# Performance work log

Measured on AMD Instinct MI355X. Metric: run time of the kernel, lower is better.

The kernel has to match this reference:

```python
import jax, jax.numpy as jnp
import numpy as np

B, S, D, H = 8, 1024, 256, 8


def setup_inputs() -> dict:
    key = jax.random.key(0)
    ks = jax.random.split(key, 8)
    scale = 0.02
    return {
        "x": jax.random.normal(ks[0], (B, S, D), dtype=jnp.float32),
        "Wq": jax.random.normal(ks[1], (H, D, D), dtype=jnp.float32) * scale,
        "Wk": jax.random.normal(ks[2], (H, D, D), dtype=jnp.float32) * scale,
        "Wv": jax.random.normal(ks[3], (H, D, D), dtype=jnp.float32) * scale,
        "bq": jax.random.normal(ks[4], (H, D), dtype=jnp.float32) * scale,
        "bk": jax.random.normal(ks[5], (H, D), dtype=jnp.float32) * scale,
        "bv": jax.random.normal(ks[6], (H, D), dtype=jnp.float32) * scale,
        "Wp": jax.random.normal(ks[7], (D, H * D), dtype=jnp.float32) * scale,
    }


def reference(x, Wq, Wk, Wv, bq, bk, bv, Wp):
    # Per-head Linear layers, vectorized over the head axis.
    # torch Linear: y = x @ W.T + b, W shape [out, in] -> einsum 'bsd,hed->bhse'
    q = jnp.einsum('bsd,hed->bhse', x, Wq) + bq[:, None, :]   # [B,H,S,D]
    k = jnp.einsum('bsd,hed->bhse', x, Wk) + bk[:, None, :]
    v = jnp.einsum('bsd,hed->bhse', x, Wv) + bv[:, None, :]
    d = x.shape[-1]
    scores = jnp.einsum('bhse,bhte->bhst', q, k) / jnp.sqrt(jnp.float32(d))
    attn = jax.nn.softmax(scores, axis=-1)                    # softmax over keys (dim=2 per head)
    o = jnp.einsum('bhst,bhte->bhse', attn, v)                # [B,H,S,D]
    # concat heads along feature dim (head order preserved)
    o = o.transpose(0, 2, 1, 3).reshape(x.shape[0], x.shape[1], -1)  # [B,S,H*D]
    return o @ Wp.T                                           # bias-free projection [B,S,D]
```

## Files before the change

kernel.cpp:

```cpp
#include <hip/hip_runtime.h>

typedef unsigned short u16;
typedef __attribute__((ext_vector_type(4)))  float f32x4;
typedef __attribute__((ext_vector_type(16))) float f32x16;
typedef __attribute__((ext_vector_type(8)))  short s16x8;
typedef __attribute__((ext_vector_type(4)))  unsigned short u16x4;

typedef const __attribute__((address_space(1))) void* gp1;
typedef __attribute__((address_space(3))) void* lp3;
#define GLOAD16(g, l) __builtin_amdgcn_global_load_lds((gp1)(g), (lp3)(l), 16, 0, 0)

__device__ __forceinline__ u16 f2bf(float f) {
    union { float f; unsigned u; } c; c.f = f;
    unsigned r = c.u + 0x7fffu + ((c.u >> 16) & 1u);
    return (u16)(r >> 16);
}

__global__ void castall(const float* __restrict__ x,  const float* __restrict__ wq,
                        const float* __restrict__ wk, const float* __restrict__ wv,
                        const float* __restrict__ wp,
                        u16* __restrict__ xb,  u16* __restrict__ wqb, u16* __restrict__ wkb,
                        u16* __restrict__ wvb, u16* __restrict__ wpb) {
    int blk = blockIdx.x;
    const float* src; u16* dst; long off;
    if (blk < 2048) { src = x; dst = xb; off = (long)blk * 1024; }
    else {
        int w = (blk - 2048) >> 9, bb = (blk - 2048) & 511;
        src = (w == 0 ? wq : w == 1 ? wk : w == 2 ? wv : wp);
        dst = (w == 0 ? wqb : w == 1 ? wkb : w == 2 ? wvb : wpb);
        off = (long)bb * 1024;
    }
    long i = off + threadIdx.x * 4;
    f32x4 v = *(const f32x4*)(src + i);
    u16x4 o;
    o[0] = f2bf(v[0]); o[1] = f2bf(v[1]); o[2] = f2bf(v[2]); o[3] = f2bf(v[3]);
    *(u16x4*)(dst + i) = o;
}

__global__ __launch_bounds__(256) void qkv_gemm(
    const u16* __restrict__ xb,
    const u16* __restrict__ Wqb, const u16* __restrict__ Wkb, const u16* __restrict__ Wvb,
    const float* __restrict__ bq, const float* __restrict__ bk, const float* __restrict__ bv,
    u16* __restrict__ Qb, u16* __restrict__ Kimg, u16* __restrict__ Vimg)
{
    __shared__ u16 As[128 * 32];
    __shared__ u16 Bs[128 * 32];
    const int tid  = threadIdx.x;
    const int lane = tid & 63;
    const int li   = lane & 15, lg = lane >> 4;
    const int wave = tid >> 6;
    const int wr   = wave >> 1, wc = wave & 1;
    const int m0   = blockIdx.x * 128;
    const int n0g  = blockIdx.y * 128;
    const int w    = n0g >> 11;
    const int h    = (n0g >> 8) & 7;
    const int e0   = n0g & 255;
    const u16* Wsel = (w == 0 ? Wqb : (w == 1 ? Wkb : Wvb)) + h * 65536;

    const int srow = tid >> 2;
    const int scol = (tid & 3) * 8;

    f32x4 acc[4][4] = {};

    for (int k0 = 0; k0 < 256; k0 += 32) {
        __syncthreads();
        #pragma unroll
        for (int i = 0; i < 2; ++i) {
            int row = i * 64 + srow;
            GLOAD16(&xb[(m0 + row) * 256 + k0 + scol],   &As[i * 2048 + tid * 8]);
            GLOAD16(&Wsel[(e0 + row) * 256 + k0 + scol], &Bs[i * 2048 + tid * 8]);
        }
        __syncthreads();
        s16x8 af[4], bf[4];
        #pragma unroll
        for (int mi = 0; mi < 4; ++mi)
            af[mi] = *(const s16x8*)&As[(wr * 64 + mi * 16 + li) * 32 + lg * 8];
        #pragma unroll
        for (int ni = 0; ni < 4; ++ni)
            bf[ni] = *(const s16x8*)&Bs[(wc * 64 + ni * 16 + li) * 32 + lg * 8];
        #pragma unroll
        for (int mi = 0; mi < 4; ++mi)
            #pragma unroll
            for (int ni = 0; ni < 4; ++ni)
                acc[mi][ni] = __builtin_amdgcn_mfma_f32_16x16x32_bf16(af[mi], bf[ni], acc[mi][ni], 0, 0, 0);
    }

    const int b  = m0 >> 10;
    const int s0 = m0 & 1023;
    if (w == 0) {
        const float* bp = bq + 256 * h;
        #pragma unroll
        for (int ni = 0; ni < 4; ++ni) {
            const int e = e0 + wc * 64 + ni * 16 + li;
            const float bias = bp[e];
            u16* obase = Qb + ((size_t)(b * 8 + h)) * 1024 * 256 + e;
            #pragma unroll
            for (int mi = 0; mi < 4; ++mi)
                #pragma unroll
                for (int r = 0; r < 4; ++r) {
                    int s = s0 + wr * 64 + mi * 16 + lg * 4 + r;
                    obase[(size_t)s * 256] = f2bf(acc[mi][ni][r] + bias);
                }
        }
    } else if (w == 1) {
        const float* bp = bk + 256 * h;
        u16* kb = Kimg + ((size_t)(b * 8 + h)) * 262144;
        #pragma unroll
        for (int ni = 0; ni < 4; ++ni) {
            const int e = e0 + wc * 64 + ni * 16 + li;
            const float bias = bp[e];
            #pragma unroll
            for (int mi = 0; mi < 4; ++mi)
                #pragma unroll
                for (int r = 0; r < 4; ++r) {
                    int s = s0 + wr * 64 + mi * 16 + lg * 4 + r;
                    int t = s >> 5, rr = s & 31;
                    size_t idx = (size_t)t * 8192 + rr * 256
                               + (((e & ~7) ^ ((rr & 7) << 3)) | (e & 7));
                    kb[idx] = f2bf(acc[mi][ni][r] + bias);
                }
        }
    } else {
        const float* bp = bv + 256 * h;
        u16* vb = Vimg + ((size_t)(b * 8 + h)) * 327680;
        #pragma unroll
        for (int ni = 0; ni < 4; ++ni) {
            const int e = e0 + wc * 64 + ni * 16 + li;
            const float bias = bp[e];
            #pragma unroll
            for (int mi = 0; mi < 4; ++mi) {
                int s = s0 + wr * 64 + mi * 16 + lg * 4;
                int t = s >> 5, cj = s & 31;
                size_t idx = (size_t)t * 10240 + e * 40 + cj;
                u16x4 pk;
                #pragma unroll
                for (int r = 0; r < 4; ++r) pk[r] = f2bf(acc[mi][ni][r] + bias);
                *(u16x4*)&vb[idx] = pk;
            }
        }
    }
}

__device__ __forceinline__ void softmax_pack(
    f32x16& sacc, float& m_run, float& l_run, f32x16* oacc,
    int hi, s16x8& paA, s16x8& paB)
{
    const float C = 0.09016844f;
    const float THR = 16.0f;
    float pm = -1e30f;
    #pragma unroll
    for (int r = 0; r < 16; ++r) pm = fmaxf(pm, sacc[r]);
    pm = fmaxf(pm, __shfl_xor(pm, 32));
    if (!__all(pm - m_run <= THR)) {
        const float mnew = fmaxf(m_run, pm);
        const float corr = __builtin_amdgcn_exp2f((m_run - mnew) * C);
        l_run *= corr;
        #pragma unroll
        for (int r = 0; r < 16; ++r) {
            float rc = __shfl(corr, (r & 3) + 8 * (r >> 2) + 4 * hi);
            #pragma unroll
            for (int et = 0; et < 8; ++et) oacc[et][r] *= rc;
        }
        m_run = mnew;
    }
    float psum = 0.f;
    #pragma unroll
    for (int r = 0; r < 16; ++r) {
        float p = __builtin_amdgcn_exp2f((sacc[r] - m_run) * C);
        psum += p;
        sacc[r] = p;
    }
    psum += __shfl_xor(psum, 32);
    l_run += psum;
    unsigned dwA[4], dwB[4];
    #pragma unroll
    for (int c = 0; c < 4; ++c) {
        asm("v_cvt_pk_bf16_f32 %0, %1, %2" : "=v"(dwA[c]) : "v"(sacc[4*c]),   "v"(sacc[4*c+1]));
        asm("v_cvt_pk_bf16_f32 %0, %1, %2" : "=v"(dwB[c]) : "v"(sacc[4*c+2]), "v"(sacc[4*c+3]));
    }
    {
        unsigned a0 = dwA[0], a1 = dwA[1], b0 = dwB[0], b1 = dwB[1];
        asm("v_permlane32_swap_b32 %0, %1" : "+v"(a0), "+v"(a1));
        asm("v_permlane32_swap_b32 %0, %1" : "+v"(b0), "+v"(b1));
        union { unsigned u[4]; s16x8 v; } pk;
        pk.u[0] = a0; pk.u[1] = b0; pk.u[2] = a1; pk.u[3] = b1;
        paA = pk.v;
    }
    {
        unsigned a0 = dwA[2], a1 = dwA[3], b0 = dwB[2], b1 = dwB[3];
        asm("v_permlane32_swap_b32 %0, %1" : "+v"(a0), "+v"(a1));
        asm("v_permlane32_swap_b32 %0, %1" : "+v"(b0), "+v"(b1));
        union { unsigned u[4]; s16x8 v; } pk;
        pk.u[0] = a0; pk.u[1] = b0; pk.u[2] = a1; pk.u[3] = b1;
        paB = pk.v;
    }
}

__global__ __launch_bounds__(512, 2) void attn(
    const u16* __restrict__ Qb, const u16* __restrict__ Kimg,
    const u16* __restrict__ Vimg, u16* __restrict__ Ob)
{
    __shared__ u16 kbuf[3][8192];
    __shared__ u16 vbuf[3][10240];
    const int tid  = threadIdx.x;
    const int lane = tid & 63;
    const int wave = tid >> 6;
    const int col  = lane & 31;
    const int hi   = lane >> 5;
    const int hi8  = hi * 8;
    const int ksw  = (lane & 7) << 3;
    const int bid  = ((blockIdx.x & 7) << 5) | (blockIdx.x >> 3);
    const int bh   = bid >> 2;
    const int qblk = bid & 3;
    const int q0   = qblk * 256 + wave * 32;

    const u16* qp = Qb + ((size_t)bh * 1024 + q0) * 256;
    const u16* kg = Kimg + (size_t)bh * 262144;
    const u16* vg = Vimg + (size_t)bh * 327680;

    #define STAGE(sl, t)                                                          \
        {                                                                         \
            const int sl_ = (sl);                                                 \
            const int t_  = (t);                                                  \
            if (tid < 256) {                                                      \
                const size_t kb_ = (size_t)t_ * 8192 + tid * 8;                   \
                _Pragma("unroll")                                                 \
                for (int c_ = 0; c_ < 4; ++c_)                                    \
                    GLOAD16(&kg[kb_ + c_ * 2048], &kbuf[sl_][c_ * 2048 + tid * 8]); \
            } else {                                                              \
                const int    vt_ = tid - 256;                                     \
                const size_t vb_ = (size_t)t_ * 10240 + vt_ * 8;                  \
                _Pragma("unroll")                                                 \
                for (int c_ = 0; c_ < 5; ++c_)                                    \
                    GLOAD16(&vg[vb_ + c_ * 2048], &vbuf[sl_][c_ * 2048 + vt_ * 8]); \
            }                                                                     \
        }

    s16x8 qf[16];
    #pragma unroll
    for (int dk = 0; dk < 16; ++dk)
        qf[dk] = *(const s16x8*)&qp[(size_t)col * 256 + dk * 16 + hi8];

    STAGE(0, 0);
    STAGE(1, 1);
    STAGE(2, 2);

    f32x16 oacc[8] = {};
    float m_run = -1e30f, l_run = 0.f;
    f32x16 sacc;
    s16x8 paA, paB;

    for (int i = 0; i < 32; ++i) {
        if (tid < 256) { asm volatile("s_waitcnt vmcnt(8)"  ::: "memory"); }
        else           { asm volatile("s_waitcnt vmcnt(10)" ::: "memory"); }
        __builtin_amdgcn_s_barrier();
        asm volatile("" ::: "memory");
        const int slot = i % 3;
        const u16* kt = kbuf[slot];
        const u16* vt = vbuf[slot];

        __builtin_amdgcn_s_setprio(1);
        {
            sacc = (f32x16){};
            const int rb_ = col * 256;
            #pragma unroll
            for (int dk_ = 0; dk_ < 16; ++dk_) {
                s16x8 kf = *(const s16x8*)&kt[rb_ + ((dk_ * 16 + hi8) ^ ksw)];
                sacc = __builtin_amdgcn_mfma_f32_32x32x16_bf16(kf, qf[dk_], sacc, 0, 0, 0);
            }
        }
        __builtin_amdgcn_s_setprio(0);

        softmax_pack(sacc, m_run, l_run, oacc, hi, paA, paB);

        __builtin_amdgcn_s_setprio(1);
        {
            #pragma unroll
            for (int et_ = 0; et_ < 8; ++et_) {
                s16x8 vf = *(const s16x8*)&vt[(et_ * 32 + col) * 40 + hi8];
                oacc[et_] = __builtin_amdgcn_mfma_f32_32x32x16_bf16(paA, vf, oacc[et_], 0, 0, 0);
            }
            #pragma unroll
            for (int et_ = 0; et_ < 8; ++et_) {
                s16x8 vf = *(const s16x8*)&vt[(et_ * 32 + col) * 40 + 16 + hi8];
                oacc[et_] = __builtin_amdgcn_mfma_f32_32x32x16_bf16(paB, vf, oacc[et_], 0, 0, 0);
            }
        }
        __builtin_amdgcn_s_setprio(0);

        asm volatile("" ::: "memory");
        __builtin_amdgcn_s_barrier();
        asm volatile("" ::: "memory");
        const int nt = (i + 3 < 32) ? (i + 3) : 31;
        STAGE(slot, nt);
    }
    #undef STAGE

    const float linv = 1.0f / l_run;
    const int b = bh >> 3, h = bh & 7;
    u16* op = Ob + ((size_t)b * 1024) * 2048 + h * 256;
    #pragma unroll
    for (int r = 0; r < 16; ++r) {
        const int crow = (r & 3) + 8 * (r >> 2) + 4 * hi;
        float lr = __shfl(linv, crow);
        const size_t row = q0 + crow;
        #pragma unroll
        for (int et = 0; et < 8; ++et)
            op[row * 2048 + et * 32 + col] = f2bf(oacc[et][r] * lr);
    }
}

__global__ __launch_bounds__(256) void out_gemm(
    const u16* __restrict__ Ob, const u16* __restrict__ Wpb, float* __restrict__ out)
{
    __shared__ u16 As[32 * 32];
    __shared__ u16 Bs[128 * 32];
    const int tid  = threadIdx.x;
    const int lane = tid & 63;
    const int li   = lane & 15, lg = lane >> 4;
    const int wave = tid >> 6;
    const int wr   = wave >> 1, wc = wave & 1;
    const int m0   = blockIdx.x * 32;
    const int n0   = blockIdx.y * 128;
    const int srow = tid >> 2;
    const int scol = (tid & 3) * 8;

    f32x4 acc[4] = {};

    for (int k0 = 0; k0 < 2048; k0 += 32) {
        __syncthreads();
        if (tid < 128)
            GLOAD16(&Ob[(size_t)(m0 + srow) * 2048 + k0 + scol], &As[tid * 8]);
        #pragma unroll
        for (int i = 0; i < 2; ++i)
            GLOAD16(&Wpb[(size_t)(n0 + i * 64 + srow) * 2048 + k0 + scol],
                    &Bs[i * 2048 + tid * 8]);
        __syncthreads();
        s16x8 af, bf[4];
        af = *(const s16x8*)&As[(wr * 16 + li) * 32 + lg * 8];
        #pragma unroll
        for (int ni = 0; ni < 4; ++ni)
            bf[ni] = *(const s16x8*)&Bs[(wc * 64 + ni * 16 + li) * 32 + lg * 8];
        #pragma unroll
        for (int ni = 0; ni < 4; ++ni)
            acc[ni] = __builtin_amdgcn_mfma_f32_16x16x32_bf16(af, bf[ni], acc[ni], 0, 0, 0);
    }

    #pragma unroll
    for (int ni = 0; ni < 4; ++ni) {
        int n = n0 + wc * 64 + ni * 16 + li;
        #pragma unroll
        for (int r = 0; r < 4; ++r) {
            int m = m0 + wr * 16 + lg * 4 + r;
            out[(size_t)m * 256 + n] = acc[ni][r];
        }
    }
}

extern "C" void kernel_launch(void* const* d_in, const int* in_sizes, int n_in,
                              void* d_out, int out_size, void* d_ws, size_t ws_size,
                              hipStream_t stream) {
    const float* x  = (const float*)d_in[0];
    const float* Wq = (const float*)d_in[1];
    const float* Wk = (const float*)d_in[2];
    const float* Wv = (const float*)d_in[3];
    const float* bq = (const float*)d_in[4];
    const float* bk = (const float*)d_in[5];
    const float* bv = (const float*)d_in[6];
    const float* Wp = (const float*)d_in[7];
    float* out = (float*)d_out;

    u16* xb   = (u16*)d_ws;
    u16* Wqb  = xb   + (1u << 21);
    u16* Wkb  = Wqb  + (1u << 19);
    u16* Wvb  = Wkb  + (1u << 19);
    u16* Wpb  = Wvb  + (1u << 19);
    u16* Qb   = Wpb  + (1u << 19);
    u16* Kimg = Qb   + (1u << 24);
    u16* Vimg = Kimg + (1u << 24);
    u16* Ob   = Vimg + 20971520u;

    castall<<<4096, 256, 0, stream>>>(x, Wq, Wk, Wv, Wp, xb, Wqb, Wkb, Wvb, Wpb);
    qkv_gemm<<<dim3(64, 48), 256, 0, stream>>>(xb, Wqb, Wkb, Wvb, bq, bk, bv, Qb, Kimg, Vimg);
    attn<<<256, 512, 0, stream>>>(Qb, Kimg, Vimg, Ob);
    out_gemm<<<dim3(256, 2), 256, 0, stream>>>(Ob, Wpb, out);
}
```

Before: 167.0 us.

## Software-pipeline attention loop so QK of tile i overlaps PV of tile i-1

Restructures the attention main loop so each iteration issues the QK^T MFMAs for the current key tile together with the PV MFMAs for the previous tile, then runs the softmax. The softmax's exp and reduction latency can then hide behind matrix work in the next iteration. K and V staging are decoupled: V lags one tile behind K in its own triple-buffer slots, and a tail step handles the last PV. The max and sum reductions in the softmax also become tree reductions to shorten dependency chains. In exchange, the loop keeps more registers live (probabilities carried across iterations) and the buffer and wait-count bookkeeping is more intricate.

```diff
diff --git a/kernel.cpp b/kernel.cpp
--- a/kernel.cpp
+++ b/kernel.cpp
@@ -147,9 +147,16 @@
 {
     const float C = 0.09016844f;
     const float THR = 16.0f;
-    float pm = -1e30f;
-    #pragma unroll
-    for (int r = 0; r < 16; ++r) pm = fmaxf(pm, sacc[r]);
+    float pm;
+    {
+        float t[8];
+        #pragma unroll
+        for (int r = 0; r < 8; ++r) t[r] = fmaxf(sacc[r], sacc[r + 8]);
+        #pragma unroll
+        for (int r = 0; r < 4; ++r) t[r] = fmaxf(t[r], t[r + 4]);
+        t[0] = fmaxf(t[0], t[2]); t[1] = fmaxf(t[1], t[3]);
+        pm = fmaxf(t[0], t[1]);
+    }
     pm = fmaxf(pm, __shfl_xor(pm, 32));
     if (!__all(pm - m_run <= THR)) {
         const float mnew = fmaxf(m_run, pm);
@@ -163,12 +170,17 @@
         }
         m_run = mnew;
     }
-    float psum = 0.f;
     #pragma unroll
-    for (int r = 0; r < 16; ++r) {
-        float p = __builtin_amdgcn_exp2f((sacc[r] - m_run) * C);
-        psum += p;
-        sacc[r] = p;
+    for (int r = 0; r < 16; ++r)
+        sacc[r] = __builtin_amdgcn_exp2f((sacc[r] - m_run) * C);
+    float psum;
+    {
+        float s[8];
+        #pragma unroll
+        for (int r = 0; r < 8; ++r) s[r] = sacc[r] + sacc[r + 8];
+        #pragma unroll
+        for (int r = 0; r < 4; ++r) s[r] = s[r] + s[r + 4];
+        psum = (s[0] + s[1]) + (s[2] + s[3]);
     }
     psum += __shfl_xor(psum, 32);
     l_run += psum;
@@ -194,6 +206,38 @@
         pk.u[0] = a0; pk.u[1] = b0; pk.u[2] = a1; pk.u[3] = b1;
         paB = pk.v;
     }
+}
+
+__device__ __forceinline__ void attn_body(
+    const int i, const u16* __restrict__ kt, const u16* __restrict__ vt,
+    const s16x8 (&qf)[16], const int col, const int hi, const int ksw,
+    f32x16* oacc, float& m_run, float& l_run, s16x8& paA, s16x8& paB)
+{
+    const int hi8 = hi * 8;
+    f32x16 sacc = (f32x16){};
+    __builtin_amdgcn_s_setprio(1);
+    {
+        const int rb_ = col * 256;
+        #pragma unroll
+        for (int dk = 0; dk < 16; ++dk) {
+            s16x8 kf = *(const s16x8*)&kt[rb_ + ((dk * 16 + hi8) ^ ksw)];
+            sacc = __builtin_amdgcn_mfma_f32_32x32x16_bf16(kf, qf[dk], sacc, 0, 0, 0);
+        }
+    }
+    if (i > 0) {
+        #pragma unroll
+        for (int et = 0; et < 8; ++et) {
+            s16x8 vf = *(const s16x8*)&vt[(et * 32 + col) * 40 + hi8];
+            oacc[et] = __builtin_amdgcn_mfma_f32_32x32x16_bf16(paA, vf, oacc[et], 0, 0, 0);
+        }
+        #pragma unroll
+        for (int et = 0; et < 8; ++et) {
+            s16x8 vf = *(const s16x8*)&vt[(et * 32 + col) * 40 + 16 + hi8];
+            oacc[et] = __builtin_amdgcn_mfma_f32_32x32x16_bf16(paB, vf, oacc[et], 0, 0, 0);
+        }
+    }
+    __builtin_amdgcn_s_setprio(0);
+    softmax_pack(sacc, m_run, l_run, oacc, hi, paA, paB);
 }
 
 __global__ __launch_bounds__(512, 2) void attn(
@@ -218,22 +262,22 @@
     const u16* kg = Kimg + (size_t)bh * 262144;
     const u16* vg = Vimg + (size_t)bh * 327680;
 
-    #define STAGE(sl, t)                                                          \
+    #define STAGEK(sl, t)                                                         \
         {                                                                         \
-            const int sl_ = (sl);                                                 \
-            const int t_  = (t);                                                  \
-            if (tid < 256) {                                                      \
-                const size_t kb_ = (size_t)t_ * 8192 + tid * 8;                   \
-                _Pragma("unroll")                                                 \
-                for (int c_ = 0; c_ < 4; ++c_)                                    \
-                    GLOAD16(&kg[kb_ + c_ * 2048], &kbuf[sl_][c_ * 2048 + tid * 8]); \
-            } else {                                                              \
-                const int    vt_ = tid - 256;                                     \
-                const size_t vb_ = (size_t)t_ * 10240 + vt_ * 8;                  \
-                _Pragma("unroll")                                                 \
-                for (int c_ = 0; c_ < 5; ++c_)                                    \
-                    GLOAD16(&vg[vb_ + c_ * 2048], &vbuf[sl_][c_ * 2048 + vt_ * 8]); \
-            }                                                                     \
+            const int s_ = (sl), t_ = (t);                                        \
+            const size_t kb_ = (size_t)t_ * 8192 + tid * 8;                       \
+            _Pragma("unroll")                                                     \
+            for (int c_ = 0; c_ < 4; ++c_)                                        \
+                GLOAD16(&kg[kb_ + c_ * 2048], &kbuf[s_][c_ * 2048 + tid * 8]);    \
+        }
+    #define STAGEV(sl, t)                                                         \
+        {                                                                         \
+            const int s_ = (sl), t_ = (t);                                        \
+            const int vth_ = tid - 256;                                          \
+            const size_t vb_ = (size_t)t_ * 10240 + vth_ * 8;                     \
+            _Pragma("unroll")                                                     \
+            for (int c_ = 0; c_ < 5; ++c_)                                        \
+                GLOAD16(&vg[vb_ + c_ * 2048], &vbuf[s_][c_ * 2048 + vth_ * 8]);   \
         }
 
     s16x8 qf[16];
@@ -241,60 +285,51 @@
     for (int dk = 0; dk < 16; ++dk)
         qf[dk] = *(const s16x8*)&qp[(size_t)col * 256 + dk * 16 + hi8];
 
-    STAGE(0, 0);
-    STAGE(1, 1);
-    STAGE(2, 2);
+    if (tid < 256) { STAGEK(0, 0); STAGEK(1, 1); STAGEK(2, 2); }
+    else           { STAGEV(0, 0); STAGEV(1, 1); }
 
     f32x16 oacc[8] = {};
     float m_run = -1e30f, l_run = 0.f;
-    f32x16 sacc;
-    s16x8 paA, paB;
+    s16x8 paA = {}, paB = {};
 
     for (int i = 0; i < 32; ++i) {
         if (tid < 256) { asm volatile("s_waitcnt vmcnt(8)"  ::: "memory"); }
         else           { asm volatile("s_waitcnt vmcnt(10)" ::: "memory"); }
         __builtin_amdgcn_s_barrier();
         asm volatile("" ::: "memory");
-        const int slot = i % 3;
-        const u16* kt = kbuf[slot];
-        const u16* vt = vbuf[slot];
-
-        __builtin_amdgcn_s_setprio(1);
-        {
-            sacc = (f32x16){};
-            const int rb_ = col * 256;
-            #pragma unroll
-            for (int dk_ = 0; dk_ < 16; ++dk_) {
-                s16x8 kf = *(const s16x8*)&kt[rb_ + ((dk_ * 16 + hi8) ^ ksw)];
-                sacc = __builtin_amdgcn_mfma_f32_32x32x16_bf16(kf, qf[dk_], sacc, 0, 0, 0);
-            }
-        }
-        __builtin_amdgcn_s_setprio(0);
-
-        softmax_pack(sacc, m_run, l_run, oacc, hi, paA, paB);
-
-        __builtin_amdgcn_s_setprio(1);
-        {
-            #pragma unroll
-            for (int et_ = 0; et_ < 8; ++et_) {
-                s16x8 vf = *(const s16x8*)&vt[(et_ * 32 + col) * 40 + hi8];
-                oacc[et_] = __builtin_amdgcn_mfma_f32_32x32x16_bf16(paA, vf, oacc[et_], 0, 0, 0);
-            }
-            #pragma unroll
-            for (int et_ = 0; et_ < 8; ++et_) {
-                s16x8 vf = *(const s16x8*)&vt[(et_ * 32 + col) * 40 + 16 + hi8];
-                oacc[et_] = __builtin_amdgcn_mfma_f32_32x32x16_bf16(paB, vf, oacc[et_], 0, 0, 0);
-            }
-        }
-        __builtin_amdgcn_s_setprio(0);
-
+        const int ks = i % 3;
+        const int vs = (i + 2) % 3;
+        attn_body(i, kbuf[ks], vbuf[vs], qf, col, hi, ksw,
+                  oacc, m_run, l_run, paA, paB);
         asm volatile("" ::: "memory");
         __builtin_amdgcn_s_barrier();
         asm volatile("" ::: "memory");
-        const int nt = (i + 3 < 32) ? (i + 3) : 31;
-        STAGE(slot, nt);
-    }
-    #undef STAGE
+        const int ktile = (i + 3 < 32) ? (i + 3) : 31;
+        const int vtile = (i + 2 < 32) ? (i + 2) : 31;
+        if (tid < 256) { STAGEK(ks, ktile); }
+        else           { STAGEV(vs, vtile); }
+    }
+    #undef STAGEK
+    #undef STAGEV
+
+    if (tid >= 256) { asm volatile("s_waitcnt vmcnt(10)" ::: "memory"); }
+    __builtin_amdgcn_s_barrier();
+    asm volatile("" ::: "memory");
+    {
+        const u16* vt = vbuf[1];
+        __builtin_amdgcn_s_setprio(1);
+        #pragma unroll
+        for (int et = 0; et < 8; ++et) {
+            s16x8 vf = *(const s16x8*)&vt[(et * 32 + col) * 40 + hi8];
+            oacc[et] = __builtin_amdgcn_mfma_f32_32x32x16_bf16(paA, vf, oacc[et], 0, 0, 0);
+        }
+        #pragma unroll
+        for (int et = 0; et < 8; ++et) {
+            s16x8 vf = *(const s16x8*)&vt[(et * 32 + col) * 40 + 16 + hi8];
+            oacc[et] = __builtin_amdgcn_mfma_f32_32x32x16_bf16(paB, vf, oacc[et], 0, 0, 0);
+        }
+        __builtin_amdgcn_s_setprio(0);
+    }
 
     const float linv = 1.0f / l_run;
     const int b = bh >> 3, h = bh & 7;
```

New measurement: 167.2 us. About the same (+0.1%).
